# Kernel tuning notes

Measured on AMD Instinct MI355X. Metric: run time of the kernel, lower is better.

Reference implementation:

```python
import jax, jax.numpy as jnp
import numpy as np

D_MODEL = 1024
N_HEADS = 16
HEAD_DIM = D_MODEL // N_HEADS


def setup_inputs() -> dict:
    key = jax.random.key(0)
    k1, k2, k3 = jax.random.split(key, 3)
    scale = 1.0 / np.sqrt(D_MODEL)
    x = jax.random.normal(k1, (4, 2048, D_MODEL), dtype=jnp.float32)
    w_qkv = jax.random.normal(k2, (D_MODEL, 3 * D_MODEL), dtype=jnp.float32) * scale
    b_qkv = jnp.zeros((3 * D_MODEL,), dtype=jnp.float32)
    w_proj = jax.random.normal(k3, (D_MODEL, D_MODEL), dtype=jnp.float32) * scale
    b_proj = jnp.zeros((D_MODEL,), dtype=jnp.float32)
    return {"x": x, "w_qkv": w_qkv, "b_qkv": b_qkv, "w_proj": w_proj, "b_proj": b_proj}


def reference(x, w_qkv, b_qkv, w_proj, b_proj):
    B, T, C = x.shape
    H, Dh = N_HEADS, HEAD_DIM
    qkv = x @ w_qkv + b_qkv                       # (B, T, 3C)
    qkv = qkv.reshape(B, T, 3, H, Dh)
    q = qkv[:, :, 0].transpose(0, 2, 1, 3)        # (B, H, T, Dh)
    k = qkv[:, :, 1].transpose(0, 2, 1, 3)
    v = qkv[:, :, 2].transpose(0, 2, 1, 3)
    att = jnp.einsum('bhqd,bhkd->bhqk', q, k) / jnp.sqrt(jnp.float32(Dh))
    causal = jnp.tril(jnp.ones((T, T), dtype=bool))
    att = jnp.where(causal[None, None], att, -jnp.inf)
    att = jax.nn.softmax(att, axis=-1)
    y = jnp.einsum('bhqk,bhkd->bhqd', att, v)     # (B, H, T, Dh)
    y = y.transpose(0, 2, 1, 3).reshape(B, T, C)
    return y @ w_proj + b_proj
```

## Files before the change

kernel.cpp:

```cpp
#include <hip/hip_runtime.h>
#include <hip/hip_bf16.h>
#include <math.h>

typedef __bf16 bf16_t;
typedef __bf16 bf16x4 __attribute__((ext_vector_type(4)));
typedef __bf16 bf16x8 __attribute__((ext_vector_type(8)));
typedef float floatx4 __attribute__((ext_vector_type(4)));
typedef unsigned int u32;

#define AS1 __attribute__((address_space(1)))
#define AS3 __attribute__((address_space(3)))

__device__ bf16_t g_xb[8192 * 1024];
__device__ bf16_t g_wqkvT[3072 * 1024];
__device__ bf16_t g_wprojT[1024 * 1024];
__device__ float  g_bqkv[3072];
__device__ float  g_bproj[1024];
__device__ bf16_t g_qkv[3ull * 64 * 2048 * 64];
#define HBREG (64ull * 2048 * 64)

__global__ __launch_bounds__(256) void cvt_x(const float* __restrict__ src,
                                             const float* __restrict__ bq,
                                             const float* __restrict__ bp) {
  int blk = blockIdx.x;
  int tid = threadIdx.x;
  if (blk < 4096) {
    int i0 = (blk * 256 + tid) * 8;
    const float4* s = (const float4*)src;
    float4 a = s[i0 / 4], b = s[i0 / 4 + 1];
    bf16x8 v;
    v[0] = (bf16_t)a.x; v[1] = (bf16_t)a.y; v[2] = (bf16_t)a.z; v[3] = (bf16_t)a.w;
    v[4] = (bf16_t)b.x; v[5] = (bf16_t)b.y; v[6] = (bf16_t)b.z; v[7] = (bf16_t)b.w;
    *(bf16x8*)&g_xb[i0] = v;
  } else if (blk == 4096) {
    for (int i = tid; i < 3072; i += 256) g_bqkv[i] = bq[i];
  } else {
    for (int i = tid; i < 1024; i += 256) g_bproj[i] = bp[i];
  }
}

__global__ __launch_bounds__(256) void tr64(const float* __restrict__ wqkv,
                                            const float* __restrict__ wproj) {
  __shared__ bf16_t tile[64][65];
  const int R = 1024;
  int bx = blockIdx.x;
  const float* in;
  bf16_t* out;
  int C, c0;
  if (bx < 48) { in = wqkv; out = g_wqkvT; C = 3072; c0 = bx * 64; }
  else         { in = wproj; out = g_wprojT; C = 1024; c0 = (bx - 48) * 64; }
  int r0 = blockIdx.y * 64;
  int tid = threadIdx.x;
#pragma unroll
  for (int it = 0; it < 16; ++it) {
    int idx = tid + it * 256;
    int r = idx >> 6, c = idx & 63;
    tile[r][c] = (bf16_t)in[(size_t)(r0 + r) * C + (c0 + c)];
  }
  __syncthreads();
#pragma unroll
  for (int it = 0; it < 16; ++it) {
    int idx = tid + it * 256;
    int r = idx >> 6, c = idx & 63;
    out[(size_t)(c0 + r) * R + (r0 + c)] = tile[c][r];
  }
}

#define MFMA16(a, b, c) __builtin_amdgcn_mfma_f32_16x16x32_bf16(a, b, c, 0, 0, 0)
#define SB0() __builtin_amdgcn_sched_barrier(0)
#define PH_MID()                                          \
  do {                                                    \
    SB0();                                                \
    __builtin_amdgcn_s_barrier();                         \
    SB0();                                                \
    asm volatile("s_waitcnt lgkmcnt(0)" ::: "memory");    \
    SB0();                                                \
  } while (0)
#define PH_END()                                          \
  do {                                                    \
    SB0();                                                \
    __builtin_amdgcn_s_barrier();                         \
    SB0();                                                \
  } while (0)

__global__ __launch_bounds__(512) void gemm256(float* __restrict__ out_ext,
                                               int M, int N, int K,
                                               int amode, int bsel, int cmode) {
  __shared__ alignas(16) bf16_t As[2][256 * 64];
  __shared__ alignas(16) bf16_t Bs[2][256 * 64];
  (void)M;
  const bf16_t* Ag = (amode == 0) ? g_xb : g_qkv;
  const bf16_t* Bt = bsel ? g_wprojT : g_wqkvT;
  const float* bias = bsel ? g_bproj : g_bqkv;
  const int tid = threadIdx.x;

  int gx = gridDim.x;
  int nwg = gx * gridDim.y;
  int lin = blockIdx.y * gx + blockIdx.x;
  int swz = (lin & 7) * (nwg >> 3) + (lin >> 3);
  int bx = swz % gx, by = swz / gx;
  const int m0 = by * 256, n0 = bx * 256;

  const int lane = tid & 63, wave = tid >> 6;
  const int wm = wave >> 2, wn = wave & 3;
  const int quad = lane >> 4, l16 = lane & 15;

  const u32 xv = (u32)(l16 & 7) << 4;
  const u32 sq0 = ((u32)quad * 16u) ^ xv;
  const u32 sq1 = (64u + (u32)quad * 16u) ^ xv;
  const u32 a_rb = (u32)(wm * 64 + l16) * 128u;
  const u32 b_rb = (u32)(wn * 32 + l16) * 128u;

  u32 row_j[2], scol_j[2];
#pragma unroll
  for (int j = 0; j < 2; ++j) {
    u32 L = ((u32)j * 512u + (u32)tid) * 16u;
    u32 y = L ^ (((L >> 7) & 7u) << 4);
    row_j[j] = y >> 7;
    scol_j[j] = (y & 127u) >> 1;
  }
  u32 a_go[2][2], b_go[2][2], akts;
  if (amode == 0) {
#pragma unroll
    for (int h = 0; h < 2; ++h)
#pragma unroll
      for (int j = 0; j < 2; ++j)
        a_go[h][j] = (u32)(m0 + h * 128 + (int)row_j[j]) * (u32)K + scol_j[j];
    akts = 64u;
  } else {
#pragma unroll
    for (int h = 0; h < 2; ++h)
#pragma unroll
      for (int j = 0; j < 2; ++j) {
        int m = m0 + h * 128 + (int)row_j[j];
        a_go[h][j] = (u32)(m >> 11) * 2097152u + (u32)(m & 2047) * 64u + scol_j[j];
      }
    akts = 131072u;
  }
#pragma unroll
  for (int h = 0; h < 2; ++h)
#pragma unroll
    for (int j = 0; j < 2; ++j)
      b_go[h][j] = (u32)(n0 + h * 128 + (int)row_j[j]) * (u32)K + scol_j[j];

  auto stageA = [&](int kt_, int h_) {
#pragma unroll
    for (int j = 0; j < 2; ++j)
      __builtin_amdgcn_global_load_lds(
          (const AS1 void*)(Ag + (size_t)(a_go[h_][j] + (u32)kt_ * akts)),
          (AS3 void*)&As[kt_ & 1][h_ * 8192 + (j * 512 + tid) * 8], 16, 0, 0);
  };
  auto stageB = [&](int kt_, int h_) {
#pragma unroll
    for (int j = 0; j < 2; ++j)
      __builtin_amdgcn_global_load_lds(
          (const AS1 void*)(Bt + (size_t)(b_go[h_][j] + (u32)kt_ * 64u)),
          (AS3 void*)&Bs[kt_ & 1][h_ * 8192 + (j * 512 + tid) * 8], 16, 0, 0);
  };

  floatx4 acc[2][4][2][2] = {};
  const int NT = K >> 6;

  stageA(0, 0); SB0(); stageB(0, 0); SB0();
  stageA(0, 1); SB0(); stageB(0, 1); SB0();
  stageA(1, 0); SB0(); stageB(1, 0); SB0();
  asm volatile("s_waitcnt vmcnt(8)" ::: "memory");
  __builtin_amdgcn_s_barrier();
  SB0();

  for (int kt = 0; kt < NT; ++kt) {
    const int b = kt & 1;
    const char* Ab = (const char*)&As[b][0];
    const char* Bb = (const char*)&Bs[b][0];
    bf16x8 af[4][2], bv[2][2], bw[2][2];

#pragma unroll
    for (int mf = 0; mf < 4; ++mf) {
      af[mf][0] = *(const bf16x8*)(Ab + (a_rb + mf * 2048 + sq0));
      af[mf][1] = *(const bf16x8*)(Ab + (a_rb + mf * 2048 + sq1));
    }
#pragma unroll
    for (int nf = 0; nf < 2; ++nf) {
      bv[nf][0] = *(const bf16x8*)(Bb + (b_rb + nf * 2048 + sq0));
      bv[nf][1] = *(const bf16x8*)(Bb + (b_rb + nf * 2048 + sq1));
    }
    if (kt + 1 < NT) stageA(kt + 1, 1);
    PH_MID();
    __builtin_amdgcn_s_setprio(1);
#pragma unroll
    for (int mf = 0; mf < 4; ++mf)
#pragma unroll
      for (int nf = 0; nf < 2; ++nf) {
        acc[0][mf][0][nf] = MFMA16(af[mf][0], bv[nf][0], acc[0][mf][0][nf]);
        acc[0][mf][0][nf] = MFMA16(af[mf][1], bv[nf][1], acc[0][mf][0][nf]);
      }
    __builtin_amdgcn_s_setprio(0);
    SB0();
    if (kt + 1 < NT) asm volatile("s_waitcnt vmcnt(6)" ::: "memory");
    else             asm volatile("s_waitcnt vmcnt(0)" ::: "memory");
    __builtin_amdgcn_s_barrier();
    SB0();

#pragma unroll
    for (int nf = 0; nf < 2; ++nf) {
      bw[nf][0] = *(const bf16x8*)(Bb + (b_rb + 16384 + nf * 2048 + sq0));
      bw[nf][1] = *(const bf16x8*)(Bb + (b_rb + 16384 + nf * 2048 + sq1));
    }
    if (kt + 1 < NT) stageB(kt + 1, 1);
    PH_MID();
    __builtin_amdgcn_s_setprio(1);
#pragma unroll
    for (int mf = 0; mf < 4; ++mf)
#pragma unroll
      for (int nf = 0; nf < 2; ++nf) {
        acc[0][mf][1][nf] = MFMA16(af[mf][0], bw[nf][0], acc[0][mf][1][nf]);
        acc[0][mf][1][nf] = MFMA16(af[mf][1], bw[nf][1], acc[0][mf][1][nf]);
      }
    __builtin_amdgcn_s_setprio(0);
    PH_END();

#pragma unroll
    for (int mf = 0; mf < 4; ++mf) {
      af[mf][0] = *(const bf16x8*)(Ab + (a_rb + 16384 + mf * 2048 + sq0));
      af[mf][1] = *(const bf16x8*)(Ab + (a_rb + 16384 + mf * 2048 + sq1));
    }
    if (kt + 2 < NT) stageA(kt + 2, 0);
    PH_MID();
    __builtin_amdgcn_s_setprio(1);
#pragma unroll
    for (int mf = 0; mf < 4; ++mf)
#pragma unroll
      for (int nf = 0; nf < 2; ++nf) {
        acc[1][mf][1][nf] = MFMA16(af[mf][0], bw[nf][0], acc[1][mf][1][nf]);
        acc[1][mf][1][nf] = MFMA16(af[mf][1], bw[nf][1], acc[1][mf][1][nf]);
      }
    __builtin_amdgcn_s_setprio(0);
    PH_END();

    if (kt + 2 < NT) stageB(kt + 2, 0);
    PH_MID();
    __builtin_amdgcn_s_setprio(1);
#pragma unroll
    for (int mf = 0; mf < 4; ++mf)
#pragma unroll
      for (int nf = 0; nf < 2; ++nf) {
        acc[1][mf][0][nf] = MFMA16(af[mf][0], bv[nf][0], acc[1][mf][0][nf]);
        acc[1][mf][0][nf] = MFMA16(af[mf][1], bv[nf][1], acc[1][mf][0][nf]);
      }
    __builtin_amdgcn_s_setprio(0);
    SB0();
    if (kt + 2 < NT)      asm volatile("s_waitcnt vmcnt(8)" ::: "memory");
    else if (kt + 1 < NT) asm volatile("s_waitcnt vmcnt(4)" ::: "memory");
    __builtin_amdgcn_s_barrier();
    SB0();
  }

#pragma unroll
  for (int mh = 0; mh < 2; ++mh)
#pragma unroll
  for (int mf = 0; mf < 4; ++mf)
#pragma unroll
  for (int nh = 0; nh < 2; ++nh)
#pragma unroll
  for (int nf = 0; nf < 2; ++nf) {
    int ncol = n0 + wn * 32 + nh * 128 + nf * 16 + l16;
    float bb = bias[ncol];
    int mbase = m0 + wm * 64 + mh * 128 + mf * 16 + quad * 4;
    if (cmode == 0) {
      int which = ncol >> 10;
      int h = (ncol >> 6) & 15;
      int d = ncol & 63;
      int b_ = mbase >> 11, t = mbase & 2047;
      if (which == 2) {
        bf16x4 pk;
#pragma unroll
        for (int r = 0; r < 4; ++r) pk[r] = (bf16_t)(acc[mh][mf][nh][nf][r] + bb);
        size_t dst = 2 * HBREG + ((size_t)((b_ * 16 + h) * 64 + d)) * 2048 + t;
        *(bf16x4*)&g_qkv[dst] = pk;
      } else {
        size_t base = (size_t)which * HBREG +
                      ((size_t)((b_ * 16 + h) * 2048 + t)) * 64 + d;
#pragma unroll
        for (int r = 0; r < 4; ++r)
          g_qkv[base + (size_t)r * 64] = (bf16_t)(acc[mh][mf][nh][nf][r] + bb);
      }
    } else {
#pragma unroll
      for (int r = 0; r < 4; ++r)
        out_ext[(size_t)(mbase + r) * N + ncol] = acc[mh][mf][nh][nf][r] + bb;
    }
  }
}

__global__ __launch_bounds__(256, 3) void attn64() {
  __shared__ bf16_t Ks[2][64 * 64];
  __shared__ bf16_t Vt[2][64 * 64];
  __shared__ bf16_t Ps[8][16 * 64];
  const float C1 = 0.1803368801111204f;
  const float C2 = -23.083120654223414f;
  const int tid = threadIdx.x;
  const int qpair = blockIdx.y;
  const int bh = blockIdx.x;
  const bf16_t* Qb  = g_qkv + (size_t)bh * 2048 * 64;
  const bf16_t* Kb  = g_qkv + HBREG + (size_t)bh * 2048 * 64;
  const bf16_t* VTb = g_qkv + 2 * HBREG + (size_t)bh * 64 * 2048;
  bf16_t* Yb = g_qkv + (size_t)bh * 2048 * 64;
  const int lane = tid & 63, wave = tid >> 6;
  const int quad = lane >> 4, l16 = lane & 15;
  const int row0 = tid >> 3, c80 = (tid & 7) * 8;
  char* PwH = (char*)&Ps[wave * 2 + 0][0];
  char* PwL = (char*)&Ps[wave * 2 + 1][0];

  const int stW0 = row0 * 128 + ((c80 * 2) ^ ((row0 & 7) << 4));
  const int stW1 = stW0 + 32 * 128;
  const int fmask = (l16 & 7) << 4;
  const int fs0 = (quad * 16) ^ fmask;
  const int fs1 = (64 + quad * 16) ^ fmask;
  int pwb[4];
#pragma unroll
  for (int tn = 0; tn < 4; ++tn)
    pwb[tn] = l16 * 128 + ((tn * 32 + quad * 8) ^ fmask);
  const int prd = l16 * 128;

  const int qlo = qpair, qhi = 31 - qpair;
  const int qrow_l = qlo * 64 + wave * 16 + l16;
  const int qrow_h = qhi * 64 + wave * 16 + l16;

  bf16x8 ones8;
#pragma unroll
  for (int j = 0; j < 8; ++j) ones8[j] = (bf16_t)1.0f;

  bf16x8 aql0 = *(const bf16x8*)&Qb[(size_t)qrow_l * 64 + quad * 8];
  bf16x8 aql1 = *(const bf16x8*)&Qb[(size_t)qrow_l * 64 + 32 + quad * 8];
  bf16x8 aqh0 = *(const bf16x8*)&Qb[(size_t)qrow_h * 64 + quad * 8];
  bf16x8 aqh1 = *(const bf16x8*)&Qb[(size_t)qrow_h * 64 + 32 + quad * 8];

  floatx4 oh[4] = {}, ol[4] = {};
  floatx4 osh = {}, osl = {};

  bf16x8 kp0 = *(const bf16x8*)&Kb[(size_t)row0 * 64 + c80];
  bf16x8 kp1 = *(const bf16x8*)&Kb[(size_t)(row0 + 32) * 64 + c80];
  bf16x8 vp0 = *(const bf16x8*)&VTb[(size_t)row0 * 2048 + c80];
  bf16x8 vp1 = *(const bf16x8*)&VTb[(size_t)(row0 + 32) * 2048 + c80];

  const int ntiles = qhi + 1;
  int c = 0;
  for (int kt = 0; kt < ntiles; ++kt) {
    char* KsB = (char*)&Ks[c][0];
    char* VtB = (char*)&Vt[c][0];
    *(bf16x8*)(KsB + stW0) = kp0;
    *(bf16x8*)(KsB + stW1) = kp1;
    *(bf16x8*)(VtB + stW0) = vp0;
    *(bf16x8*)(VtB + stW1) = vp1;
    if (kt + 1 < ntiles) {
      const int k1 = (kt + 1) * 64;
      kp0 = *(const bf16x8*)&Kb[(size_t)(k1 + row0) * 64 + c80];
      kp1 = *(const bf16x8*)&Kb[(size_t)(k1 + row0 + 32) * 64 + c80];
      vp0 = *(const bf16x8*)&VTb[(size_t)row0 * 2048 + k1 + c80];
      vp1 = *(const bf16x8*)&VTb[(size_t)(row0 + 32) * 2048 + k1 + c80];
    }
    __syncthreads();

    const bool lo_on = (kt <= qlo);
    const int k0 = kt * 64;

    bf16x8 bk0[4], bk1[4];
#pragma unroll
    for (int tn = 0; tn < 4; ++tn) {
      int rb = (tn * 16 + l16) * 128;
      bk0[tn] = *(const bf16x8*)(KsB + rb + fs0);
      bk1[tn] = *(const bf16x8*)(KsB + rb + fs1);
    }

    floatx4 sh[4], sl[4];
    __builtin_amdgcn_s_setprio(1);
#pragma unroll
    for (int tn = 0; tn < 4; ++tn) {
      floatx4 z = {};
      z = __builtin_amdgcn_mfma_f32_16x16x32_bf16(bk0[tn], aqh0, z, 0, 0, 0);
      z = __builtin_amdgcn_mfma_f32_16x16x32_bf16(bk1[tn], aqh1, z, 0, 0, 0);
      sh[tn] = z;
    }
    if (lo_on) {
#pragma unroll
      for (int tn = 0; tn < 4; ++tn) {
        floatx4 z = {};
        z = __builtin_amdgcn_mfma_f32_16x16x32_bf16(bk0[tn], aql0, z, 0, 0, 0);
        z = __builtin_amdgcn_mfma_f32_16x16x32_bf16(bk1[tn], aql1, z, 0, 0, 0);
        sl[tn] = z;
      }
    }
    __builtin_amdgcn_s_setprio(0);

    bf16x8 av0[4], av1[4];
#pragma unroll
    for (int tn = 0; tn < 4; ++tn) {
      int rb = (tn * 16 + l16) * 128;
      av0[tn] = *(const bf16x8*)(VtB + rb + fs0);
      av1[tn] = *(const bf16x8*)(VtB + rb + fs1);
    }

    if (kt == qhi) {
#pragma unroll
      for (int tn = 0; tn < 4; ++tn)
#pragma unroll
        for (int r = 0; r < 4; ++r) {
          int kcol = k0 + tn * 16 + quad * 4 + r;
          float p = exp2f(fminf(fmaf(sh[tn][r], C1, C2), 30.f));
          sh[tn][r] = (kcol > qrow_h) ? 0.f : p;
        }
    } else {
#pragma unroll
      for (int tn = 0; tn < 4; ++tn)
#pragma unroll
        for (int r = 0; r < 4; ++r)
          sh[tn][r] = exp2f(fminf(fmaf(sh[tn][r], C1, C2), 30.f));
    }
#pragma unroll
    for (int tn = 0; tn < 4; ++tn) {
      bf16x4 pk;
#pragma unroll
      for (int r = 0; r < 4; ++r) pk[r] = (bf16_t)sh[tn][r];
      *(bf16x4*)(PwH + pwb[tn]) = pk;
    }

    if (lo_on) {
      if (kt == qlo) {
#pragma unroll
        for (int tn = 0; tn < 4; ++tn)
#pragma unroll
          for (int r = 0; r < 4; ++r) {
            int kcol = k0 + tn * 16 + quad * 4 + r;
            float p = exp2f(fminf(fmaf(sl[tn][r], C1, C2), 30.f));
            sl[tn][r] = (kcol > qrow_l) ? 0.f : p;
          }
      } else {
#pragma unroll
        for (int tn = 0; tn < 4; ++tn)
#pragma unroll
          for (int r = 0; r < 4; ++r)
            sl[tn][r] = exp2f(fminf(fmaf(sl[tn][r], C1, C2), 30.f));
      }
#pragma unroll
      for (int tn = 0; tn < 4; ++tn) {
        bf16x4 pk;
#pragma unroll
        for (int r = 0; r < 4; ++r) pk[r] = (bf16_t)sl[tn][r];
        *(bf16x4*)(PwL + pwb[tn]) = pk;
      }
    }

    bf16x8 pph0 = *(const bf16x8*)(PwH + prd + fs0);
    bf16x8 pph1 = *(const bf16x8*)(PwH + prd + fs1);
    __builtin_amdgcn_s_setprio(1);
#pragma unroll
    for (int tn = 0; tn < 4; ++tn) {
      oh[tn] = __builtin_amdgcn_mfma_f32_16x16x32_bf16(av0[tn], pph0, oh[tn], 0, 0, 0);
      oh[tn] = __builtin_amdgcn_mfma_f32_16x16x32_bf16(av1[tn], pph1, oh[tn], 0, 0, 0);
    }
    osh = __builtin_amdgcn_mfma_f32_16x16x32_bf16(ones8, pph0, osh, 0, 0, 0);
    osh = __builtin_amdgcn_mfma_f32_16x16x32_bf16(ones8, pph1, osh, 0, 0, 0);
    __builtin_amdgcn_s_setprio(0);

    if (lo_on) {
      bf16x8 ppl0 = *(const bf16x8*)(PwL + prd + fs0);
      bf16x8 ppl1 = *(const bf16x8*)(PwL + prd + fs1);
      __builtin_amdgcn_s_setprio(1);
#pragma unroll
      for (int tn = 0; tn < 4; ++tn) {
        ol[tn] = __builtin_amdgcn_mfma_f32_16x16x32_bf16(av0[tn], ppl0, ol[tn], 0, 0, 0);
        ol[tn] = __builtin_amdgcn_mfma_f32_16x16x32_bf16(av1[tn], ppl1, ol[tn], 0, 0, 0);
      }
      osl = __builtin_amdgcn_mfma_f32_16x16x32_bf16(ones8, ppl0, osl, 0, 0, 0);
      osl = __builtin_amdgcn_mfma_f32_16x16x32_bf16(ones8, ppl1, osl, 0, 0, 0);
      __builtin_amdgcn_s_setprio(0);
    }
    c ^= 1;
  }

  float invh = 1.0f / osh[0];
#pragma unroll
  for (int tn = 0; tn < 4; ++tn) {
    bf16x4 yv;
#pragma unroll
    for (int r = 0; r < 4; ++r) yv[r] = (bf16_t)(oh[tn][r] * invh);
    *(bf16x4*)&Yb[(size_t)qrow_h * 64 + tn * 16 + quad * 4] = yv;
  }
  float invl = 1.0f / osl[0];
#pragma unroll
  for (int tn = 0; tn < 4; ++tn) {
    bf16x4 yv;
#pragma unroll
    for (int r = 0; r < 4; ++r) yv[r] = (bf16_t)(ol[tn][r] * invl);
    *(bf16x4*)&Yb[(size_t)qrow_l * 64 + tn * 16 + quad * 4] = yv;
  }
}

extern "C" void kernel_launch(void* const* d_in, const int* in_sizes, int n_in,
                              void* d_out, int out_size, void* d_ws, size_t ws_size,
                              hipStream_t stream) {
  const float* x      = (const float*)d_in[0];
  const float* w_qkv  = (const float*)d_in[1];
  const float* b_qkv  = (const float*)d_in[2];
  const float* w_proj = (const float*)d_in[3];
  const float* b_proj = (const float*)d_in[4];
  (void)d_ws; (void)ws_size;

  cvt_x<<<4098, 256, 0, stream>>>(x, b_qkv, b_proj);
  tr64<<<dim3(64, 16), 256, 0, stream>>>(w_qkv, w_proj);

  gemm256<<<dim3(12, 32), 512, 0, stream>>>(nullptr, 8192, 3072, 1024, 0, 0, 0);

  attn64<<<dim3(64, 16), 256, 0, stream>>>();

  gemm256<<<dim3(4, 32), 512, 0, stream>>>((float*)d_out, 8192, 1024, 1024, 1, 1, 1);
}
```

Measured before the change: 285.5 us.

## Halve GEMM K-tile to 32 and rework LDS staging pipeline with occupancy hint

The 256x256 GEMM now uses a K-step of 32 instead of 64. That halves the LDS footprint to 64KB, and launch_bounds(512,4) is added to ask for more resident blocks. The LDS swizzle, the global-to-LDS load mapping and the wait/barrier schedule are rewritten for two MFMA phases per tile instead of four. The goal is better occupancy and shorter phases, at the cost of twice as many barriers per K and smaller loads per stage. The launch-bounds hint may also force register spilling given the 64 accumulators.

```diff
diff --git a/kernel.cpp b/kernel.cpp
--- a/kernel.cpp
+++ b/kernel.cpp
@@ -76,18 +76,12 @@
     asm volatile("s_waitcnt lgkmcnt(0)" ::: "memory");    \
     SB0();                                                \
   } while (0)
-#define PH_END()                                          \
-  do {                                                    \
-    SB0();                                                \
-    __builtin_amdgcn_s_barrier();                         \
-    SB0();                                                \
-  } while (0)
-
-__global__ __launch_bounds__(512) void gemm256(float* __restrict__ out_ext,
-                                               int M, int N, int K,
-                                               int amode, int bsel, int cmode) {
-  __shared__ alignas(16) bf16_t As[2][256 * 64];
-  __shared__ alignas(16) bf16_t Bs[2][256 * 64];
+
+__global__ __launch_bounds__(512, 4) void gemm256(float* __restrict__ out_ext,
+                                                  int M, int N, int K,
+                                                  int amode, int bsel, int cmode) {
+  __shared__ alignas(16) bf16_t As[2][256 * 32];
+  __shared__ alignas(16) bf16_t Bs[2][256 * 32];
   (void)M;
   const bf16_t* Ag = (amode == 0) ? g_xb : g_qkv;
   const bf16_t* Bt = bsel ? g_wprojT : g_wqkvT;
@@ -105,154 +99,104 @@
   const int wm = wave >> 2, wn = wave & 3;
   const int quad = lane >> 4, l16 = lane & 15;
 
-  const u32 xv = (u32)(l16 & 7) << 4;
-  const u32 sq0 = ((u32)quad * 16u) ^ xv;
-  const u32 sq1 = (64u + (u32)quad * 16u) ^ xv;
-  const u32 a_rb = (u32)(wm * 64 + l16) * 128u;
-  const u32 b_rb = (u32)(wn * 32 + l16) * 128u;
-
-  u32 row_j[2], scol_j[2];
+  const int ar2 = l16 >> 1, ar1 = l16 & 1;
+  const u32 FOFF = (u32)ar2 * 128u +
+                   ((((u32)ar1 * 64u) + (u32)quad * 16u) ^ ((u32)ar2 << 4));
+  const u32 a_fb = (u32)(wm * 64) * 64u + FOFF;
+  const u32 b_fb = (u32)(wn * 32) * 64u + FOFF;
+
+  const int s0_ = (tid & 7) ^ ((tid >> 3) & 7);
+  const int sr0 = (tid >> 3) * 2 + (s0_ >> 2);
+  const int scol = (s0_ & 3) * 8;
+  u32 a_go[2], b_go[2];
 #pragma unroll
   for (int j = 0; j < 2; ++j) {
-    u32 L = ((u32)j * 512u + (u32)tid) * 16u;
-    u32 y = L ^ (((L >> 7) & 7u) << 4);
-    row_j[j] = y >> 7;
-    scol_j[j] = (y & 127u) >> 1;
-  }
-  u32 a_go[2][2], b_go[2][2], akts;
-  if (amode == 0) {
-#pragma unroll
-    for (int h = 0; h < 2; ++h)
-#pragma unroll
-      for (int j = 0; j < 2; ++j)
-        a_go[h][j] = (u32)(m0 + h * 128 + (int)row_j[j]) * (u32)K + scol_j[j];
-    akts = 64u;
-  } else {
-#pragma unroll
-    for (int h = 0; h < 2; ++h)
-#pragma unroll
-      for (int j = 0; j < 2; ++j) {
-        int m = m0 + h * 128 + (int)row_j[j];
-        a_go[h][j] = (u32)(m >> 11) * 2097152u + (u32)(m & 2047) * 64u + scol_j[j];
-      }
-    akts = 131072u;
-  }
-#pragma unroll
-  for (int h = 0; h < 2; ++h)
-#pragma unroll
-    for (int j = 0; j < 2; ++j)
-      b_go[h][j] = (u32)(n0 + h * 128 + (int)row_j[j]) * (u32)K + scol_j[j];
-
-  auto stageA = [&](int kt_, int h_) {
-#pragma unroll
-    for (int j = 0; j < 2; ++j)
-      __builtin_amdgcn_global_load_lds(
-          (const AS1 void*)(Ag + (size_t)(a_go[h_][j] + (u32)kt_ * akts)),
-          (AS3 void*)&As[kt_ & 1][h_ * 8192 + (j * 512 + tid) * 8], 16, 0, 0);
+    int row = j * 128 + sr0;
+    if (amode == 0) {
+      a_go[j] = (u32)(m0 + row) * (u32)K + (u32)scol;
+    } else {
+      int m = m0 + row;
+      a_go[j] = (u32)(m >> 11) * 2097152u + (u32)(m & 2047) * 64u + (u32)scol;
+    }
+    b_go[j] = (u32)(n0 + row) * (u32)K + (u32)scol;
+  }
+
+  auto stA = [&](int kt_, int j_) {
+    u32 off = (amode == 0) ? (u32)kt_ * 32u
+                           : ((u32)(kt_ >> 1) * 131072u + (u32)(kt_ & 1) * 32u);
+    __builtin_amdgcn_global_load_lds(
+        (const AS1 void*)(Ag + (size_t)(a_go[j_] + off)),
+        (AS3 void*)&As[kt_ & 1][j_ * 4096 + tid * 8], 16, 0, 0);
   };
-  auto stageB = [&](int kt_, int h_) {
-#pragma unroll
-    for (int j = 0; j < 2; ++j)
-      __builtin_amdgcn_global_load_lds(
-          (const AS1 void*)(Bt + (size_t)(b_go[h_][j] + (u32)kt_ * 64u)),
-          (AS3 void*)&Bs[kt_ & 1][h_ * 8192 + (j * 512 + tid) * 8], 16, 0, 0);
+  auto stB = [&](int kt_, int j_) {
+    __builtin_amdgcn_global_load_lds(
+        (const AS1 void*)(Bt + (size_t)(b_go[j_] + (u32)kt_ * 32u)),
+        (AS3 void*)&Bs[kt_ & 1][j_ * 4096 + tid * 8], 16, 0, 0);
   };
 
   floatx4 acc[2][4][2][2] = {};
-  const int NT = K >> 6;
-
-  stageA(0, 0); SB0(); stageB(0, 0); SB0();
-  stageA(0, 1); SB0(); stageB(0, 1); SB0();
-  stageA(1, 0); SB0(); stageB(1, 0); SB0();
-  asm volatile("s_waitcnt vmcnt(8)" ::: "memory");
+  const int NT = K >> 5;
+
+  stA(0, 0); SB0(); stB(0, 0); SB0(); stB(0, 1); SB0(); stA(0, 1); SB0();
+  stA(1, 0); SB0(); stB(1, 0); SB0(); stB(1, 1); SB0();
+  asm volatile("s_waitcnt vmcnt(4)" ::: "memory");
   __builtin_amdgcn_s_barrier();
   SB0();
 
-  for (int kt = 0; kt < NT; ++kt) {
-    const int b = kt & 1;
+  for (int t = 0; t < NT; ++t) {
+    const int b = t & 1;
     const char* Ab = (const char*)&As[b][0];
     const char* Bb = (const char*)&Bs[b][0];
-    bf16x8 af[4][2], bv[2][2], bw[2][2];
-
-#pragma unroll
-    for (int mf = 0; mf < 4; ++mf) {
-      af[mf][0] = *(const bf16x8*)(Ab + (a_rb + mf * 2048 + sq0));
-      af[mf][1] = *(const bf16x8*)(Ab + (a_rb + mf * 2048 + sq1));
-    }
-#pragma unroll
-    for (int nf = 0; nf < 2; ++nf) {
-      bv[nf][0] = *(const bf16x8*)(Bb + (b_rb + nf * 2048 + sq0));
-      bv[nf][1] = *(const bf16x8*)(Bb + (b_rb + nf * 2048 + sq1));
-    }
-    if (kt + 1 < NT) stageA(kt + 1, 1);
+    bf16x8 af[4], bfr[2][2];
+
+#pragma unroll
+    for (int mf = 0; mf < 4; ++mf)
+      af[mf] = *(const bf16x8*)(Ab + (a_fb + mf * 1024));
+#pragma unroll
+    for (int nh = 0; nh < 2; ++nh)
+#pragma unroll
+      for (int nf = 0; nf < 2; ++nf)
+        bfr[nh][nf] = *(const bf16x8*)(Bb + (b_fb + nh * 8192 + nf * 1024));
+    if (t + 1 < NT) stA(t + 1, 1);
     PH_MID();
     __builtin_amdgcn_s_setprio(1);
 #pragma unroll
     for (int mf = 0; mf < 4; ++mf)
 #pragma unroll
-      for (int nf = 0; nf < 2; ++nf) {
-        acc[0][mf][0][nf] = MFMA16(af[mf][0], bv[nf][0], acc[0][mf][0][nf]);
-        acc[0][mf][0][nf] = MFMA16(af[mf][1], bv[nf][1], acc[0][mf][0][nf]);
-      }
+      for (int nh = 0; nh < 2; ++nh)
+#pragma unroll
+        for (int nf = 0; nf < 2; ++nf)
+          acc[0][mf][nh][nf] = MFMA16(af[mf], bfr[nh][nf], acc[0][mf][nh][nf]);
     __builtin_amdgcn_s_setprio(0);
     SB0();
-    if (kt + 1 < NT) asm volatile("s_waitcnt vmcnt(6)" ::: "memory");
-    else             asm volatile("s_waitcnt vmcnt(0)" ::: "memory");
+    if (t + 1 < NT) asm volatile("s_waitcnt vmcnt(4)" ::: "memory");
+    else            asm volatile("s_waitcnt vmcnt(0)" ::: "memory");
     __builtin_amdgcn_s_barrier();
     SB0();
 
 #pragma unroll
-    for (int nf = 0; nf < 2; ++nf) {
-      bw[nf][0] = *(const bf16x8*)(Bb + (b_rb + 16384 + nf * 2048 + sq0));
-      bw[nf][1] = *(const bf16x8*)(Bb + (b_rb + 16384 + nf * 2048 + sq1));
-    }
-    if (kt + 1 < NT) stageB(kt + 1, 1);
+    for (int mf = 0; mf < 4; ++mf)
+      af[mf] = *(const bf16x8*)(Ab + (a_fb + 8192 + mf * 1024));
+    if (t + 2 < NT) { stA(t + 2, 0); SB0(); stB(t + 2, 0); SB0(); stB(t + 2, 1); }
     PH_MID();
     __builtin_amdgcn_s_setprio(1);
 #pragma unroll
     for (int mf = 0; mf < 4; ++mf)
 #pragma unroll
-      for (int nf = 0; nf < 2; ++nf) {
-        acc[0][mf][1][nf] = MFMA16(af[mf][0], bw[nf][0], acc[0][mf][1][nf]);
-        acc[0][mf][1][nf] = MFMA16(af[mf][1], bw[nf][1], acc[0][mf][1][nf]);
-      }
+      for (int nh = 0; nh < 2; ++nh)
+#pragma unroll
+        for (int nf = 0; nf < 2; ++nf)
+          acc[1][mf][nh][nf] = MFMA16(af[mf], bfr[nh][nf], acc[1][mf][nh][nf]);
     __builtin_amdgcn_s_setprio(0);
-    PH_END();
-
-#pragma unroll
-    for (int mf = 0; mf < 4; ++mf) {
-      af[mf][0] = *(const bf16x8*)(Ab + (a_rb + 16384 + mf * 2048 + sq0));
-      af[mf][1] = *(const bf16x8*)(Ab + (a_rb + 16384 + mf * 2048 + sq1));
-    }
-    if (kt + 2 < NT) stageA(kt + 2, 0);
-    PH_MID();
-    __builtin_amdgcn_s_setprio(1);
-#pragma unroll
-    for (int mf = 0; mf < 4; ++mf)
-#pragma unroll
-      for (int nf = 0; nf < 2; ++nf) {
-        acc[1][mf][1][nf] = MFMA16(af[mf][0], bw[nf][0], acc[1][mf][1][nf]);
-        acc[1][mf][1][nf] = MFMA16(af[mf][1], bw[nf][1], acc[1][mf][1][nf]);
-      }
-    __builtin_amdgcn_s_setprio(0);
-    PH_END();
-
-    if (kt + 2 < NT) stageB(kt + 2, 0);
-    PH_MID();
-    __builtin_amdgcn_s_setprio(1);
-#pragma unroll
-    for (int mf = 0; mf < 4; ++mf)
-#pragma unroll
-      for (int nf = 0; nf < 2; ++nf) {
-        acc[1][mf][0][nf] = MFMA16(af[mf][0], bv[nf][0], acc[1][mf][0][nf]);
-        acc[1][mf][0][nf] = MFMA16(af[mf][1], bv[nf][1], acc[1][mf][0][nf]);
-      }
-    __builtin_amdgcn_s_setprio(0);
-    SB0();
-    if (kt + 2 < NT)      asm volatile("s_waitcnt vmcnt(8)" ::: "memory");
-    else if (kt + 1 < NT) asm volatile("s_waitcnt vmcnt(4)" ::: "memory");
-    __builtin_amdgcn_s_barrier();
-    SB0();
+    if (t + 1 < NT) {
+      SB0();
+      int nwait = ((t + 1 < NT) ? 1 : 0) + ((t + 2 < NT) ? 3 : 0);
+      if (nwait == 4)      asm volatile("s_waitcnt vmcnt(4)" ::: "memory");
+      else if (nwait == 1) asm volatile("s_waitcnt vmcnt(1)" ::: "memory");
+      else                 asm volatile("s_waitcnt vmcnt(0)" ::: "memory");
+      __builtin_amdgcn_s_barrier();
+      SB0();
+    }
   }
 
 #pragma unroll
```

New measurement: 822.3 us. +188.1%, slower.
